# Performance work log

Measured on AMD Instinct MI355X. Metric: run time of the kernel, lower is better.

Reference implementation:

```python
import jax, jax.numpy as jnp
import numpy as np

N, E, G, D, H, EMB, L = 200000, 3200000, 4096, 64, 64, 128, 3


def setup_inputs() -> dict:
    key = jax.random.key(0)
    ks = jax.random.split(key, 16)
    s = 0.05
    inp = {}
    inp["x_a"] = jax.random.normal(ks[0], (N, D), jnp.float32)
    inp["edge_index"] = jax.random.randint(ks[1], (2, E), 0, N)
    inp["batch"] = jnp.sort(jax.random.randint(ks[2], (N,), 0, G))
    inp["acid_idx"] = jax.random.randint(ks[3], (G,), 0, 2)
    inp["concentration"] = jax.random.uniform(ks[4], (G,), jnp.float32)
    inp["num_graphs"] = G
    # GIN MLP params per layer (input_dim_a == hl_size == 64, so stackable)
    inp["W1s"] = jax.random.normal(ks[5], (L, D, H), jnp.float32) * s
    inp["b1s"] = jnp.zeros((L, H), jnp.float32)
    inp["gammas"] = jnp.ones((L, H), jnp.float32)
    inp["betas"] = jnp.zeros((L, H), jnp.float32)
    inp["bn_means"] = jnp.zeros((L, H), jnp.float32)   # eval-mode running stats
    inp["bn_vars"] = jnp.ones((L, H), jnp.float32)
    inp["W2s"] = jax.random.normal(ks[6], (L, H, H), jnp.float32) * s
    inp["b2s"] = jnp.zeros((L, H), jnp.float32)
    inp["emb_acid"] = jax.random.normal(ks[7], (2, EMB), jnp.float32)
    inp["emb_conc"] = jax.random.normal(ks[8], (2, EMB), jnp.float32)
    FC_IN = H * L + 2 * EMB  # 448
    inp["fc1_W"] = jax.random.normal(ks[9], (FC_IN, H), jnp.float32) * s
    inp["fc1_b"] = jnp.zeros((H,), jnp.float32)
    inp["fc2_W"] = jax.random.normal(ks[10], (H, 2), jnp.float32) * s
    inp["fc2_b"] = jnp.zeros((2,), jnp.float32)
    return inp


def reference(x_a, edge_index, batch, acid_idx, concentration, num_graphs,
              W1s, b1s, gammas, betas, bn_means, bn_vars, W2s, b2s,
              emb_acid, emb_conc, fc1_W, fc1_b, fc2_W, fc2_b):
    src, dst = edge_index[0], edge_index[1]
    n_nodes = x_a.shape[0]
    x = x_a
    pooled = []
    for l in range(W1s.shape[0]):  # structurally distinct layers (params differ)
        # GINConv, eps=0: MLP(x + sum_{j->i} x_j)
        agg = jax.ops.segment_sum(x[src], dst, num_segments=n_nodes)
        h = x + agg
        h = h @ W1s[l] + b1s[l]
        # BatchNorm1d in eval mode (running stats)
        h = (h - bn_means[l]) * jax.lax.rsqrt(bn_vars[l] + 1e-5) * gammas[l] + betas[l]
        h = jax.nn.relu(h)
        h = jax.nn.relu(h @ W2s[l] + b2s[l])
        x = h  # dropout inactive at eval
        pooled.append(jax.ops.segment_sum(x, batch, num_segments=num_graphs))
    xg = jnp.concatenate(pooled, axis=1)  # [G, L*H]
    conc_idx = jnp.where(concentration == 0.5, 0, 1)
    feat = jnp.concatenate([xg, emb_acid[acid_idx], emb_conc[conc_idx]], axis=1)
    h = jax.nn.relu(feat @ fc1_W + fc1_b)  # dropout inactive at eval
    out = jax.nn.sigmoid(h @ fc2_W + fc2_b)
    return out
```

## Files before the change

### kernel.cpp

```cpp
#include <hip/hip_runtime.h>
#include <math.h>


static __device__ __forceinline__ float rlf(float v, int k) {
    return __int_as_float(__builtin_amdgcn_readlane(__float_as_int(v), k));
}
static __device__ __forceinline__ int rli(int v, int k) {
    return __builtin_amdgcn_readlane(v, k);
}


__global__ void k_hist(const int* __restrict__ dst, int* __restrict__ deg, int E) {
    int i = blockIdx.x * blockDim.x + threadIdx.x;
    int stride = gridDim.x * blockDim.x;
    for (; i < E; i += stride) atomicAdd(&deg[dst[i]], 1);
}

#define SCAN_B 512

__global__ void k_scan1(const int* __restrict__ deg, int* __restrict__ ex,
                        int* __restrict__ bsum, int n) {
    __shared__ int s[SCAN_B];
    int t = threadIdx.x;
    int i = blockIdx.x * SCAN_B + t;
    int v = (i < n) ? deg[i] : 0;
    s[t] = v;
    __syncthreads();
    for (int off = 1; off < SCAN_B; off <<= 1) {
        int tv = (t >= off) ? s[t - off] : 0;
        __syncthreads();
        s[t] += tv;
        __syncthreads();
    }
    if (i < n) ex[i] = s[t] - v;
    if (t == SCAN_B - 1) bsum[blockIdx.x] = s[t];
}

__global__ void k_scan2(int* __restrict__ bsum, int nb) {
    __shared__ int s[SCAN_B];
    int t = threadIdx.x;
    int v = (t < nb) ? bsum[t] : 0;
    s[t] = v;
    __syncthreads();
    for (int off = 1; off < SCAN_B; off <<= 1) {
        int tv = (t >= off) ? s[t - off] : 0;
        __syncthreads();
        s[t] += tv;
        __syncthreads();
    }
    if (t < nb) bsum[t] = s[t] - v;
}

__global__ void k_scan3(int* __restrict__ ex, const int* __restrict__ bsum,
                        int n, int E) {
    int i = blockIdx.x * SCAN_B + threadIdx.x;
    if (i < n) ex[i] += bsum[blockIdx.x];
    if (blockIdx.x == 0 && threadIdx.x == 0) ex[n] = E;
}

__global__ void k_scatter(const int* __restrict__ src, const int* __restrict__ dst,
                          const int* __restrict__ row_start, int* __restrict__ cur,
                          int* __restrict__ csr, int E) {
    int i = blockIdx.x * blockDim.x + threadIdx.x;
    int stride = gridDim.x * blockDim.x;
    for (; i < E; i += stride) {
        int d = dst[i];
        int p = atomicAdd(&cur[d], 1);
        csr[row_start[d] + p] = src[i];
    }
}

__global__ void k_gstart(const int* __restrict__ batch, int* __restrict__ gs,
                         int n, int G) {
    int g = blockIdx.x * blockDim.x + threadIdx.x;
    if (g > G) return;
    if (g == G) { gs[G] = n; return; }
    int lo = 0, hi = n;
    while (lo < hi) {
        int mid = (lo + hi) >> 1;
        if (batch[mid] < g) lo = mid + 1; else hi = mid;
    }
    gs[g] = lo;
}

__global__ void k_wt(const float* __restrict__ W, float* __restrict__ Wt, int total) {
    int i = blockIdx.x * blockDim.x + threadIdx.x;
    if (i >= total) return;
    int l = i >> 12, r = i & 4095, j = r >> 6, k = r & 63;
    Wt[(l << 12) + (j << 6) + k] = W[(l << 12) + (k << 6) + j];
}


__global__ __launch_bounds__(256) void k_gather(
    const float* __restrict__ x, const int* __restrict__ row_start,
    const int* __restrict__ csr, float* __restrict__ agg, int n)
{
    int lane = threadIdx.x & 63;
    int wid = (blockIdx.x * blockDim.x + threadIdx.x) >> 6;
    int nw = (gridDim.x * blockDim.x) >> 6;
    for (int node = wid; node < n; node += nw) {
        float acc = x[(size_t)node * 64 + lane];
        int s0 = row_start[node], s1 = row_start[node + 1];
        for (int base = s0; base < s1; base += 64) {
            int cnt = min(64, s1 - base);
            int idx = csr[base + (lane < cnt ? lane : 0)];
            for (int j = 0; j < cnt; j += 8) {
                float s = 0.f;
#pragma unroll
                for (int u = 0; u < 8; ++u) {
                    int jc = (j + u < cnt) ? (j + u) : (cnt - 1);
                    float a = x[(size_t)rli(idx, jc) * 64 + lane];
                    s += (j + u < cnt) ? a : 0.f;
                }
                acc += s;
            }
        }
        agg[(size_t)node * 64 + lane] = acc;
    }
}


__global__ __launch_bounds__(256, 2) void k_gemm(
    float* __restrict__ xb,
    const float* __restrict__ Wt1, const float* __restrict__ b1,
    const float* __restrict__ gamma, const float* __restrict__ beta,
    const float* __restrict__ mean, const float* __restrict__ var,
    const float* __restrict__ Wt2, const float* __restrict__ b2, int n)
{
    int lane = threadIdx.x & 63;
    int wid = (blockIdx.x * blockDim.x + threadIdx.x) >> 6;
    int nw = (gridDim.x * blockDim.x) >> 6;

    float4 w1v[16], w2v[16];
    const float4* W1p = (const float4*)Wt1 + (size_t)lane * 16;
    const float4* W2p = (const float4*)Wt2 + (size_t)lane * 16;
#pragma unroll
    for (int q = 0; q < 16; ++q) w1v[q] = W1p[q];
#pragma unroll
    for (int q = 0; q < 16; ++q) w2v[q] = W2p[q];
#pragma unroll
    for (int q = 0; q < 16; ++q) {
        asm volatile("" : "+v"(w1v[q].x), "+v"(w1v[q].y), "+v"(w1v[q].z), "+v"(w1v[q].w));
        asm volatile("" : "+v"(w2v[q].x), "+v"(w2v[q].y), "+v"(w2v[q].z), "+v"(w2v[q].w));
    }
    const float* w1 = (const float*)w1v;
    const float* w2 = (const float*)w2v;

    float bias1 = b1[lane];
    float sc = gamma[lane] * rsqrtf(var[lane] + 1e-5f);
    float sh = beta[lane] - mean[lane] * sc;
    float bias2 = b2[lane];

    for (int node = wid; node < n; node += nw) {
        float a = xb[(size_t)node * 64 + lane];
        float h0 = bias1, h1 = 0.f;
#pragma unroll
        for (int k = 0; k < 64; k += 2) {
            h0 += rlf(a, k)     * w1[k];
            h1 += rlf(a, k + 1) * w1[k + 1];
        }
        float h = fmaxf((h0 + h1) * sc + sh, 0.f);
        float o0 = bias2, o1 = 0.f;
#pragma unroll
        for (int k = 0; k < 64; k += 2) {
            o0 += rlf(h, k)     * w2[k];
            o1 += rlf(h, k + 1) * w2[k + 1];
        }
        xb[(size_t)node * 64 + lane] = fmaxf(o0 + o1, 0.f);
    }
}


__global__ __launch_bounds__(256) void k_pool(const float* __restrict__ x,
                                              const int* __restrict__ gs,
                                              float* __restrict__ pooled,
                                              int G, int l, int lh) {
    int lane = threadIdx.x & 63;
    int wid = (blockIdx.x * blockDim.x + threadIdx.x) >> 6;
    if (wid >= G) return;
    int s0 = gs[wid], s1 = gs[wid + 1];
    float a0 = 0, a1 = 0, a2 = 0, a3 = 0;
    int nd = s0;
    for (; nd + 4 <= s1; nd += 4) {
        a0 += x[(size_t)(nd + 0) * 64 + lane];
        a1 += x[(size_t)(nd + 1) * 64 + lane];
        a2 += x[(size_t)(nd + 2) * 64 + lane];
        a3 += x[(size_t)(nd + 3) * 64 + lane];
    }
    for (; nd < s1; ++nd) a0 += x[(size_t)nd * 64 + lane];
    pooled[(size_t)wid * lh + l * 64 + lane] = (a0 + a1) + (a2 + a3);
}


__global__ __launch_bounds__(256) void k_fc(
    const float* __restrict__ pooled, const int* __restrict__ acid,
    const float* __restrict__ conc, const float* __restrict__ emb_acid,
    const float* __restrict__ emb_conc, const float* __restrict__ fc1W,
    const float* __restrict__ fc1b, const float* __restrict__ fc2W,
    const float* __restrict__ fc2b, float* __restrict__ out, int G, int lh)
{
    __shared__ float sf[4][448];
    int lane = threadIdx.x & 63;
    int w = threadIdx.x >> 6;
    int g = blockIdx.x * 4 + w;
    int fcin = lh + 256;
    if (g < G) {
        const float* pr = pooled + (size_t)g * lh;
        for (int c = lane; c < lh; c += 64) sf[w][c] = pr[c];
        const float* ea = emb_acid + acid[g] * 128;
        int ci = (conc[g] == 0.5f) ? 0 : 1;
        const float* ec = emb_conc + ci * 128;
        sf[w][lh + lane] = ea[lane];
        sf[w][lh + 64 + lane] = ea[lane + 64];
        sf[w][lh + 128 + lane] = ec[lane];
        sf[w][lh + 192 + lane] = ec[lane + 64];
    }
    __syncthreads();
    if (g >= G) return;
    float h0 = fc1b[lane], h1 = 0.f;
    for (int k = 0; k + 2 <= fcin; k += 2) {
        h0 += sf[w][k] * fc1W[(size_t)k * 64 + lane];
        h1 += sf[w][k + 1] * fc1W[(size_t)(k + 1) * 64 + lane];
    }
    float h = fmaxf(h0 + h1, 0.f);
    float p0 = h * fc2W[lane * 2 + 0];
    float p1 = h * fc2W[lane * 2 + 1];
    for (int off = 32; off; off >>= 1) {
        p0 += __shfl_xor(p0, off, 64);
        p1 += __shfl_xor(p1, off, 64);
    }
    if (lane == 0) {
        out[g * 2 + 0] = 1.0f / (1.0f + expf(-(p0 + fc2b[0])));
        out[g * 2 + 1] = 1.0f / (1.0f + expf(-(p1 + fc2b[1])));
    }
}


extern "C" void kernel_launch(void* const* d_in, const int* in_sizes, int n_in,
                              void* d_out, int out_size, void* d_ws, size_t ws_size,
                              hipStream_t stream)
{
    const float* x_a      = (const float*)d_in[0];
    const int*   ei       = (const int*)d_in[1];
    const int*   batch    = (const int*)d_in[2];
    const int*   acid     = (const int*)d_in[3];
    const float* conc     = (const float*)d_in[4];
    const float* W1s      = (const float*)d_in[6];
    const float* b1s      = (const float*)d_in[7];
    const float* gammas   = (const float*)d_in[8];
    const float* betas    = (const float*)d_in[9];
    const float* bn_means = (const float*)d_in[10];
    const float* bn_vars  = (const float*)d_in[11];
    const float* W2s      = (const float*)d_in[12];
    const float* b2s      = (const float*)d_in[13];
    const float* emb_acid = (const float*)d_in[14];
    const float* emb_conc = (const float*)d_in[15];
    const float* fc1W     = (const float*)d_in[16];
    const float* fc1b     = (const float*)d_in[17];
    const float* fc2W     = (const float*)d_in[18];
    const float* fc2b     = (const float*)d_in[19];

    const int N = in_sizes[0] / 64;
    const int E = in_sizes[1] / 2;
    const int G = in_sizes[3];
    const int L = in_sizes[6] / (64 * 64);
    const int LH = 64 * L;

    char* ws = (char*)d_ws;
    size_t off = 0;
    auto alloc = [&](size_t bytes) -> void* {
        void* p = ws + off;
        off += (bytes + 255) & ~(size_t)255;
        return p;
    };
    float* buf0      = (float*)alloc((size_t)N * 64 * 4);
    float* buf1      = (float*)alloc((size_t)N * 64 * 4);
    float* pooled    = (float*)alloc((size_t)G * LH * 4);
    int*   row_start = (int*)alloc((size_t)(N + 1) * 4);
    int*   deg       = (int*)alloc((size_t)N * 4);
    int*   csr       = (int*)alloc((size_t)E * 4);
    int*   bsum      = (int*)alloc(4096);
    int*   gs        = (int*)alloc((size_t)(G + 1) * 4);
    float* Wt1       = (float*)alloc((size_t)L * 4096 * 4);
    float* Wt2       = (float*)alloc((size_t)L * 4096 * 4);

    const int* srcv = ei;
    const int* dstv = ei + E;

    hipMemsetAsync(deg, 0, (size_t)N * 4, stream);
    k_hist<<<4096, 256, 0, stream>>>(dstv, deg, E);
    int nb = (N + SCAN_B - 1) / SCAN_B;
    k_scan1<<<nb, SCAN_B, 0, stream>>>(deg, row_start, bsum, N);
    k_scan2<<<1, SCAN_B, 0, stream>>>(bsum, nb);
    k_scan3<<<nb, SCAN_B, 0, stream>>>(row_start, bsum, N, E);
    hipMemsetAsync(deg, 0, (size_t)N * 4, stream);
    k_scatter<<<4096, 256, 0, stream>>>(srcv, dstv, row_start, deg, csr, E);
    k_gstart<<<(G + 256) / 256, 256, 0, stream>>>(batch, gs, N, G);

    int wtot = L * 4096;
    k_wt<<<(wtot + 255) / 256, 256, 0, stream>>>(W1s, Wt1, wtot);
    k_wt<<<(wtot + 255) / 256, 256, 0, stream>>>(W2s, Wt2, wtot);

    const float* xin = x_a;
    float* bufs[2] = {buf0, buf1};
    for (int l = 0; l < L; ++l) {
        float* xb = bufs[l & 1];
        k_gather<<<4096, 256, 0, stream>>>(xin, row_start, csr, xb, N);
        k_gemm<<<2048, 256, 0, stream>>>(
            xb, Wt1 + (size_t)l * 4096, b1s + l * 64,
            gammas + l * 64, betas + l * 64,
            bn_means + l * 64, bn_vars + l * 64,
            Wt2 + (size_t)l * 4096, b2s + l * 64, N);
        k_pool<<<(G + 3) / 4, 256, 0, stream>>>(xb, gs, pooled, G, l, LH);
        xin = xb;
    }

    k_fc<<<(G + 3) / 4, 256, 0, stream>>>(pooled, acid, conc, emb_acid, emb_conc,
                                          fc1W, fc1b, fc2W, fc2b,
                                          (float*)d_out, G, LH);
}
```

Baseline: 1.185 ms.

## Fuse neighbor gather with GIN MLP and split CSR scatter into range passes

```diff
diff --git a/kernel.cpp b/kernel.cpp
--- a/kernel.cpp
+++ b/kernel.cpp
@@ -58,15 +58,17 @@
     if (blockIdx.x == 0 && threadIdx.x == 0) ex[n] = E;
 }
 
-__global__ void k_scatter(const int* __restrict__ src, const int* __restrict__ dst,
-                          const int* __restrict__ row_start, int* __restrict__ cur,
-                          int* __restrict__ csr, int E) {
+__global__ void k_scatter_r(const int* __restrict__ src, const int* __restrict__ dst,
+                            const int* __restrict__ row_start, int* __restrict__ cur,
+                            int* __restrict__ csr, int E, int lo, int hi) {
     int i = blockIdx.x * blockDim.x + threadIdx.x;
     int stride = gridDim.x * blockDim.x;
     for (; i < E; i += stride) {
         int d = dst[i];
-        int p = atomicAdd(&cur[d], 1);
-        csr[row_start[d] + p] = src[i];
+        if (d >= lo && d < hi) {
+            int p = atomicAdd(&cur[d], 1);
+            csr[row_start[d] + p] = src[i];
+        }
     }
 }
 
@@ -91,45 +93,18 @@
 }
 
 
-__global__ __launch_bounds__(256) void k_gather(
+__global__ __launch_bounds__(256, 2) void k_layer(
     const float* __restrict__ x, const int* __restrict__ row_start,
-    const int* __restrict__ csr, float* __restrict__ agg, int n)
+    const int* __restrict__ csr,
+    const float* __restrict__ Wt1, const float* __restrict__ b1,
+    const float* __restrict__ gamma, const float* __restrict__ beta,
+    const float* __restrict__ mean, const float* __restrict__ var,
+    const float* __restrict__ Wt2, const float* __restrict__ b2,
+    float* __restrict__ xout, int n)
 {
     int lane = threadIdx.x & 63;
     int wid = (blockIdx.x * blockDim.x + threadIdx.x) >> 6;
     int nw = (gridDim.x * blockDim.x) >> 6;
-    for (int node = wid; node < n; node += nw) {
-        float acc = x[(size_t)node * 64 + lane];
-        int s0 = row_start[node], s1 = row_start[node + 1];
-        for (int base = s0; base < s1; base += 64) {
-            int cnt = min(64, s1 - base);
-            int idx = csr[base + (lane < cnt ? lane : 0)];
-            for (int j = 0; j < cnt; j += 8) {
-                float s = 0.f;
-#pragma unroll
-                for (int u = 0; u < 8; ++u) {
-                    int jc = (j + u < cnt) ? (j + u) : (cnt - 1);
-                    float a = x[(size_t)rli(idx, jc) * 64 + lane];
-                    s += (j + u < cnt) ? a : 0.f;
-                }
-                acc += s;
-            }
-        }
-        agg[(size_t)node * 64 + lane] = acc;
-    }
-}
-
-
-__global__ __launch_bounds__(256, 2) void k_gemm(
-    float* __restrict__ xb,
-    const float* __restrict__ Wt1, const float* __restrict__ b1,
-    const float* __restrict__ gamma, const float* __restrict__ beta,
-    const float* __restrict__ mean, const float* __restrict__ var,
-    const float* __restrict__ Wt2, const float* __restrict__ b2, int n)
-{
-    int lane = threadIdx.x & 63;
-    int wid = (blockIdx.x * blockDim.x + threadIdx.x) >> 6;
-    int nw = (gridDim.x * blockDim.x) >> 6;
 
     float4 w1v[16], w2v[16];
     const float4* W1p = (const float4*)Wt1 + (size_t)lane * 16;
@@ -152,21 +127,52 @@
     float bias2 = b2[lane];
 
     for (int node = wid; node < n; node += nw) {
-        float a = xb[(size_t)node * 64 + lane];
-        float h0 = bias1, h1 = 0.f;
-#pragma unroll
-        for (int k = 0; k < 64; k += 2) {
-            h0 += rlf(a, k)     * w1[k];
-            h1 += rlf(a, k + 1) * w1[k + 1];
-        }
-        float h = fmaxf((h0 + h1) * sc + sh, 0.f);
-        float o0 = bias2, o1 = 0.f;
-#pragma unroll
-        for (int k = 0; k < 64; k += 2) {
-            o0 += rlf(h, k)     * w2[k];
+        float acc = x[(size_t)node * 64 + lane];
+        int s0 = row_start[node], s1 = row_start[node + 1];
+        int j = s0;
+        for (; j + 16 <= s1; j += 16) {
+            int idx = csr[j + (lane & 15)];
+            float t0 = 0.f, t1 = 0.f, t2 = 0.f, t3 = 0.f;
+#pragma unroll
+            for (int u = 0; u < 16; u += 4) {
+                float a0 = x[(size_t)rli(idx, u + 0) * 64 + lane];
+                float a1 = x[(size_t)rli(idx, u + 1) * 64 + lane];
+                float a2 = x[(size_t)rli(idx, u + 2) * 64 + lane];
+                float a3 = x[(size_t)rli(idx, u + 3) * 64 + lane];
+                t0 += a0; t1 += a1; t2 += a2; t3 += a3;
+            }
+            acc += (t0 + t1) + (t2 + t3);
+        }
+        int cnt = s1 - j;
+        if (cnt) {
+            int idx = csr[j + (lane & 15)];
+            float s = 0.f;
+#pragma unroll
+            for (int u = 0; u < 16; ++u) {
+                int jc = (u < cnt) ? u : 0;
+                float a = x[(size_t)rli(idx, jc) * 64 + lane];
+                s += (u < cnt) ? a : 0.f;
+            }
+            acc += s;
+        }
+        float h0 = bias1, h1 = 0.f, h2 = 0.f, h3 = 0.f;
+#pragma unroll
+        for (int k = 0; k < 64; k += 4) {
+            h0 += rlf(acc, k + 0) * w1[k + 0];
+            h1 += rlf(acc, k + 1) * w1[k + 1];
+            h2 += rlf(acc, k + 2) * w1[k + 2];
+            h3 += rlf(acc, k + 3) * w1[k + 3];
+        }
+        float h = fmaxf(((h0 + h1) + (h2 + h3)) * sc + sh, 0.f);
+        float o0 = bias2, o1 = 0.f, o2 = 0.f, o3 = 0.f;
+#pragma unroll
+        for (int k = 0; k < 64; k += 4) {
+            o0 += rlf(h, k + 0) * w2[k + 0];
             o1 += rlf(h, k + 1) * w2[k + 1];
-        }
-        xb[(size_t)node * 64 + lane] = fmaxf(o0 + o1, 0.f);
+            o2 += rlf(h, k + 2) * w2[k + 2];
+            o3 += rlf(h, k + 3) * w2[k + 3];
+        }
+        xout[(size_t)node * 64 + lane] = fmaxf((o0 + o1) + (o2 + o3), 0.f);
     }
 }
 
@@ -294,7 +300,12 @@
     k_scan2<<<1, SCAN_B, 0, stream>>>(bsum, nb);
     k_scan3<<<nb, SCAN_B, 0, stream>>>(row_start, bsum, N, E);
     hipMemsetAsync(deg, 0, (size_t)N * 4, stream);
-    k_scatter<<<4096, 256, 0, stream>>>(srcv, dstv, row_start, deg, csr, E);
+    const int NPASS = 4;
+    for (int p = 0; p < NPASS; ++p) {
+        int lo = (int)((long long)N * p / NPASS);
+        int hi = (int)((long long)N * (p + 1) / NPASS);
+        k_scatter_r<<<4096, 256, 0, stream>>>(srcv, dstv, row_start, deg, csr, E, lo, hi);
+    }
     k_gstart<<<(G + 256) / 256, 256, 0, stream>>>(batch, gs, N, G);
 
     int wtot = L * 4096;
@@ -305,12 +316,13 @@
     float* bufs[2] = {buf0, buf1};
     for (int l = 0; l < L; ++l) {
         float* xb = bufs[l & 1];
-        k_gather<<<4096, 256, 0, stream>>>(xin, row_start, csr, xb, N);
-        k_gemm<<<2048, 256, 0, stream>>>(
-            xb, Wt1 + (size_t)l * 4096, b1s + l * 64,
+        k_layer<<<2048, 256, 0, stream>>>(
+            xin, row_start, csr,
+            Wt1 + (size_t)l * 4096, b1s + l * 64,
             gammas + l * 64, betas + l * 64,
             bn_means + l * 64, bn_vars + l * 64,
-            Wt2 + (size_t)l * 4096, b2s + l * 64, N);
+            Wt2 + (size_t)l * 4096, b2s + l * 64,
+            xb, N);
         k_pool<<<(G + 3) / 4, 256, 0, stream>>>(xb, gs, pooled, G, l, LH);
         xin = xb;
     }
```

Measured after the change: 1.474 ms. 1.24x slower.
